# Optimization experiments

Measured on AMD Instinct MI355X. Metric: run time of the kernel, lower is better.

Reference implementation:

```python
import jax, jax.numpy as jnp
import numpy as np

N_NODES = 100000
N_EDGES = 1600000
IN_NODE = 129
HID = 128
N_LAYERS = 3


def setup_inputs() -> dict:
    key = jax.random.key(0)
    ks = jax.random.split(key, 20)
    gnn_in = IN_NODE - 1
    x = jax.random.normal(ks[0], (N_NODES, IN_NODE), dtype=jnp.float32)
    edge_index = jax.random.randint(ks[1], (2, N_EDGES), 0, N_NODES, dtype=jnp.int64)
    edge_attr = jax.random.uniform(ks[2], (N_EDGES, 1), dtype=jnp.float32)
    # conv layer params: lin (in->hid) per layer, scalar edge mlp per layer
    dims = [gnn_in] + [HID] * N_LAYERS
    conv_W, conv_b, edge_w = [], [], []
    for i in range(N_LAYERS):
        fin = dims[i]
        s = 1.0 / np.sqrt(fin)
        conv_W.append(jax.random.uniform(ks[3 + i], (fin, HID), jnp.float32, -s, s))
        conv_b.append(jax.random.uniform(ks[6 + i], (HID,), jnp.float32, -s, s))
        edge_w.append(jax.random.uniform(ks[9 + i], (1, 1), jnp.float32, -1.0, 1.0))
    h2 = HID // 2
    t_h = IN_NODE // 2
    s1 = 1.0 / np.sqrt(HID + 1)
    s2 = 1.0 / np.sqrt(h2)
    s3 = 1.0 / np.sqrt(IN_NODE)
    s4 = 1.0 / np.sqrt(t_h)
    return {
        "x": x, "edge_index": edge_index, "edge_attr": edge_attr,
        "conv_W": tuple(conv_W), "conv_b": tuple(conv_b), "edge_w": tuple(edge_w),
        "lin1_W": jax.random.uniform(ks[12], (HID + 1, h2), jnp.float32, -s1, s1),
        "lin1_b": jax.random.uniform(ks[13], (h2,), jnp.float32, -s1, s1),
        "lin2_W": jax.random.uniform(ks[14], (h2, 1), jnp.float32, -s2, s2),
        "lin2_b": jax.random.uniform(ks[15], (1,), jnp.float32, -s2, s2),
        "t1_W": jax.random.uniform(ks[16], (IN_NODE, t_h), jnp.float32, -s3, s3),
        "t1_b": jax.random.uniform(ks[17], (t_h,), jnp.float32, -s3, s3),
        "t2_W": jax.random.uniform(ks[18], (t_h, 1), jnp.float32, -s4, s4),
        "t2_b": jax.random.uniform(ks[19], (1,), jnp.float32, -s4, s4),
    }


def reference(x, edge_index, edge_attr, conv_W, conv_b, edge_w,
              lin1_W, lin1_b, lin2_W, lin2_b, t1_W, t1_b, t2_W, t2_b):
    n = x.shape[0]
    # add self loops with edge_attr fill_value = 1.0
    loops = jnp.arange(n, dtype=edge_index.dtype)
    src = jnp.concatenate([edge_index[0], loops])
    tgt = jnp.concatenate([edge_index[1], loops])
    ea = jnp.concatenate([edge_attr, jnp.ones((n, 1), edge_attr.dtype)], axis=0)  # [E+N,1]
    # in-degree for mean aggregation (>=1 because of self loops)
    deg = jax.ops.segment_sum(jnp.ones_like(ea[:, 0]), tgt, num_segments=n)[:, None]
    # treatment head (eval mode: no dropout)
    t = jax.nn.relu(x @ t1_W + t1_b)
    t = jax.nn.sigmoid(t @ t2_W + t2_b)  # [N,1]
    h = x[:, 1:]
    for W, b, w in zip(conv_W, conv_b, edge_w):
        ht = h @ W + b                          # [N,HID]
        gate = jax.nn.sigmoid(ea * w[0, 0])     # [E+N,1]
        msg = gate * ht[src]                    # gather + gate
        agg = jax.ops.segment_sum(msg, tgt, num_segments=n) / deg
        h = jax.nn.relu(agg)
    z = jnp.concatenate([h, t], axis=1)          # [N,HID+1]
    z = jax.nn.relu(z @ lin1_W + lin1_b)
    out = jax.nn.sigmoid(z @ lin2_W + lin2_b)[:, 0]  # [N]
    return out
```

## Files before the change

### kernel.cpp

```cpp
#include <hip/hip_runtime.h>
#include <hip/hip_fp16.h>
#include <math.h>


typedef _Float16 f16x8 __attribute__((ext_vector_type(8)));
typedef float f32x4 __attribute__((ext_vector_type(4)));

#define CNT_STRIDE 32

__device__ __forceinline__ float sigmoidf_(float v) { return 1.f / (1.f + expf(-v)); }

__global__ void sentinel_kernel(float* __restrict__ out, int n, float val) {
  int i = blockIdx.x * 256 + threadIdx.x;
  if (i < n) out[i] = val;
}

__global__ void init_kernel(const int* __restrict__ ei, int* __restrict__ flag,
                            int* __restrict__ counts, int n) {
  int i = blockIdx.x * 256 + threadIdx.x;
  if (i < (n + 1) * CNT_STRIDE) counts[i] = 0;
  if (i == 0) {
    int all0 = 1;
    for (int k = 1; k < 512; k += 2) {
      if (ei[k] != 0) { all0 = 0; break; }
    }
    *flag = all0;
  }
}

__global__ void rank_kernel(const int* __restrict__ ei, int E, int n,
                            const int* __restrict__ flag,
                            int* __restrict__ slot, int* __restrict__ counts) {
  int e = blockIdx.x * blockDim.x + threadIdx.x;
  if (e >= E) return;
  int t;
  if (*flag) {
    t = (int)((const long long*)ei)[(size_t)E + e];
  } else {
    t = ei[(size_t)E + e];
  }
  slot[e] = ((unsigned)t < (unsigned)n) ? atomicAdd(&counts[(size_t)t * CNT_STRIDE], 1) : -1;
}

__global__ void scan1_kernel(const int* __restrict__ counts, int n,
                             int* __restrict__ starts, int* __restrict__ bsums) {
  __shared__ int tmp[256];
  int i = blockIdx.x * 256 + threadIdx.x;
  int v = (i <= n) ? counts[(size_t)i * CNT_STRIDE] : 0;
  tmp[threadIdx.x] = v;
  __syncthreads();
  for (int off = 1; off < 256; off <<= 1) {
    int t = (threadIdx.x >= (unsigned)off) ? tmp[threadIdx.x - off] : 0;
    __syncthreads();
    tmp[threadIdx.x] += t;
    __syncthreads();
  }
  if (i <= n) starts[i] = tmp[threadIdx.x] - v;
  if (threadIdx.x == 255) bsums[blockIdx.x] = tmp[255];
}

__global__ void scan2_kernel(int* __restrict__ bsums, int nb) {
  __shared__ int tmp[512];
  int v = (threadIdx.x < (unsigned)nb) ? bsums[threadIdx.x] : 0;
  tmp[threadIdx.x] = v;
  __syncthreads();
  for (int off = 1; off < 512; off <<= 1) {
    int t = (threadIdx.x >= (unsigned)off) ? tmp[threadIdx.x - off] : 0;
    __syncthreads();
    tmp[threadIdx.x] += t;
    __syncthreads();
  }
  if (threadIdx.x < (unsigned)nb) bsums[threadIdx.x] = tmp[threadIdx.x] - v;
}

__global__ void scatter_kernel(const int* __restrict__ ei, const int* __restrict__ slot,
                               const int* __restrict__ starts,
                               const int* __restrict__ bsums,
                               const float* __restrict__ ea, int E, int n,
                               const int* __restrict__ flag,
                               const float* __restrict__ w0p,
                               const float* __restrict__ w1p,
                               const float* __restrict__ w2p,
                               uint2* __restrict__ csr) {
  float w0 = w0p[0], w1 = w1p[0], w2 = w2p[0];
  int f64 = *flag;
  const long long* e64 = (const long long*)ei;
  int base = blockIdx.x * blockDim.x + threadIdx.x;
  int stride = gridDim.x * blockDim.x;
#pragma unroll
  for (int u = 0; u < 4; u++) {
    int e = base + u * stride;
    if (e < E) {
      int sl = slot[e];
      if (sl >= 0) {
        int s, t;
        if (f64) {
          s = (int)e64[e];
          t = (int)e64[(size_t)E + e];
        } else {
          s = ei[e];
          t = ei[(size_t)E + e];
        }
        int pos = starts[t] + bsums[t >> 8] + sl;
        if ((unsigned)pos < (unsigned)E) {
          float a = ea[e];
          unsigned sn = (unsigned)min(max(s, 0), min(n - 1, 0x1ffff));
          unsigned g0 = (unsigned)__float2uint_rn(sigmoidf_(a * w0) * 32767.f);
          unsigned g1 = (unsigned)__float2uint_rn(sigmoidf_(a * w1) * 32767.f);
          unsigned g2 = (unsigned)__float2uint_rn(sigmoidf_(a * w2) * 32767.f);
          csr[pos] = make_uint2(sn | (g0 << 17), g1 | (g2 << 15));
        }
      }
    }
  }
}

__global__ void slice_kernel(const float* __restrict__ x, _Float16* __restrict__ h,
                             float* __restrict__ x0, int n) {
  int idx = blockIdx.x * blockDim.x + threadIdx.x;
  if (idx < n * 128) {
    int node = idx >> 7;
    int k = idx & 127;
    h[idx] = (_Float16)x[(size_t)node * 129 + 1 + k];
  }
  if (idx < n) x0[idx] = x[(size_t)idx * 129];
}

__global__ __launch_bounds__(256) void head_mfma_kernel(const _Float16* __restrict__ h,
    const float* __restrict__ extra, const float* __restrict__ W1,
    const float* __restrict__ b1, const float* __restrict__ w2,
    const float* __restrict__ b2, float* __restrict__ out, int n,
    int hrow0, int xrow) {
  __shared__ __align__(16) _Float16 sB[4 * 4 * 64 * 8];
  __shared__ float sWx[64], sB1[64], sW2[64];
  for (int idx = threadIdx.x; idx < 8192; idx += 256) {
    int k = idx >> 6, col = idx & 63;
    float w = W1[(size_t)(hrow0 + k) * 64 + col];
    int ks = k >> 5, quad = (k >> 3) & 3, j = k & 7;
    int nt = col >> 4, cl = col & 15;
    sB[(((ks * 4 + nt) * 64) + quad * 16 + cl) * 8 + j] = (_Float16)w;
  }
  if (threadIdx.x < 64) {
    sWx[threadIdx.x] = W1[(size_t)xrow * 64 + threadIdx.x];
    sB1[threadIdx.x] = b1[threadIdx.x];
    sW2[threadIdx.x] = w2[threadIdx.x];
  }
  __syncthreads();
  int wv = threadIdx.x >> 6, lane = threadIdx.x & 63;
  int quad = lane >> 4, l15 = lane & 15;
  int n0 = (blockIdx.x * 4 + wv) * 16;
  if (n0 >= n) return;
  int node_a = min(n0 + l15, n - 1);
  const _Float16* hrow = h + (size_t)node_a * 128 + quad * 8;

  f32x4 acc[4];
#pragma unroll
  for (int t = 0; t < 4; t++) acc[t] = (f32x4){0.f, 0.f, 0.f, 0.f};
  for (int ks = 0; ks < 4; ks++) {
    f16x8 afrag = *(const f16x8*)(hrow + ks * 32);
    const f16x8* bp = (const f16x8*)sB;
#pragma unroll
    for (int t = 0; t < 4; t++) {
      f16x8 bfrag = bp[(ks * 4 + t) * 64 + lane];
      acc[t] = __builtin_amdgcn_mfma_f32_16x16x32_f16(afrag, bfrag, acc[t], 0, 0, 0);
    }
  }
  float b2v = b2[0];
  float xv[4], part[4] = {0.f, 0.f, 0.f, 0.f};
#pragma unroll
  for (int r = 0; r < 4; r++) xv[r] = extra[min(n0 + quad * 4 + r, n - 1)];
#pragma unroll
  for (int t = 0; t < 4; t++) {
    int col = t * 16 + l15;
    float wx = sWx[col], bb = sB1[col], w2v = sW2[col];
#pragma unroll
    for (int r = 0; r < 4; r++) {
      float u = fmaxf(acc[t][r] + xv[r] * wx + bb, 0.f);
      part[r] += u * w2v;
    }
  }
#pragma unroll
  for (int r = 0; r < 4; r++) {
    float p = part[r];
    p += __shfl_xor(p, 1); p += __shfl_xor(p, 2);
    p += __shfl_xor(p, 4); p += __shfl_xor(p, 8);
    int node = n0 + quad * 4 + r;
    if (l15 == 0 && node < n) out[node] = sigmoidf_(p + b2v);
  }
}

__global__ __launch_bounds__(256) void gemm_mfma_kernel(const _Float16* __restrict__ h,
    const float* __restrict__ Wg, const float* __restrict__ b,
    _Float16* __restrict__ out16, int n) {
  __shared__ __align__(16) _Float16 sB[4 * 8 * 64 * 8];
  for (int i = threadIdx.x; i < 4096; i += 256) {
    int k = i >> 5;
    int n4 = (i & 31) * 4;
    float4 w4 = ((const float4*)Wg)[i];
    int ks = k >> 5, quad = (k >> 3) & 3, j = k & 7;
#pragma unroll
    for (int c = 0; c < 4; c++) {
      int col = n4 + c;
      int nt = col >> 4, cl = col & 15;
      sB[(((ks * 8 + nt) * 64) + quad * 16 + cl) * 8 + j] =
          (_Float16)((const float*)&w4)[c];
    }
  }
  __syncthreads();
  int wv = threadIdx.x >> 6, lane = threadIdx.x & 63;
  int quad = lane >> 4, l15 = lane & 15;
  int tiles = (n + 63) >> 6;
  for (int tile = blockIdx.x; tile < tiles; tile += gridDim.x) {
    int n0 = (tile * 4 + wv) * 16;
    if (n0 >= n) continue;
    int node_a = min(n0 + l15, n - 1);
    const _Float16* hrow = h + (size_t)node_a * 128 + quad * 8;

    f32x4 acc[8];
#pragma unroll
    for (int t = 0; t < 8; t++) acc[t] = (f32x4){0.f, 0.f, 0.f, 0.f};

    for (int ks = 0; ks < 4; ks++) {
      f16x8 afrag = *(const f16x8*)(hrow + ks * 32);
      const f16x8* bp = (const f16x8*)(sB + ks * 8 * 64 * 8);
#pragma unroll
      for (int t = 0; t < 8; t++) {
        f16x8 bfrag = bp[t * 64 + lane];
        acc[t] = __builtin_amdgcn_mfma_f32_16x16x32_f16(afrag, bfrag, acc[t], 0, 0, 0);
      }
    }
#pragma unroll
    for (int t = 0; t < 8; t++) {
      float bias = b[t * 16 + l15];
#pragma unroll
      for (int r = 0; r < 4; r++) {
        int node = n0 + quad * 4 + r;
        if (node < n)
          out16[(size_t)node * 128 + t * 16 + l15] = (_Float16)(acc[t][r] + bias);
      }
    }
  }
}

template <int LAYER>
__device__ __forceinline__ float gate_(uint2 r) {
  const float inv = 1.f / 32767.f;
  if (LAYER == 0) return (float)(r.x >> 17) * inv;
  if (LAYER == 1) return (float)(r.y & 0x7fffu) * inv;
  return (float)(r.y >> 15) * inv;
}

template <int LAYER>
__global__ __launch_bounds__(256) void agg_kernel(const __half2* __restrict__ ht,
    const uint2* __restrict__ csr, const int* __restrict__ starts,
    const int* __restrict__ bsums, const float* __restrict__ wp,
    __half2* __restrict__ hout, int n) {
  int wv = threadIdx.x >> 6, lane = threadIdx.x & 63;
  int node = blockIdx.x * 4 + wv;
  if (node >= n) return;
  int s = starts[node] + bsums[node >> 8];
  int c = starts[node + 1] + bsums[(node + 1) >> 8] - s;
  float gs = sigmoidf_(wp[0]);
  const __half2* htl = ht + lane;
  float2 v0 = __half22float2(htl[(size_t)node << 6]);
  float ax = gs * v0.x, ay = gs * v0.y;
  float bx = 0.f, by = 0.f;
  int j = 0;
  for (; j + 8 <= c; j += 8) {
    uint2 r0 = csr[s + j],     r1 = csr[s + j + 1];
    uint2 r2 = csr[s + j + 2], r3 = csr[s + j + 3];
    uint2 r4 = csr[s + j + 4], r5 = csr[s + j + 5];
    uint2 r6 = csr[s + j + 6], r7 = csr[s + j + 7];
    __half2 h0 = htl[(size_t)(r0.x & 0x1ffffu) << 6];
    __half2 h1 = htl[(size_t)(r1.x & 0x1ffffu) << 6];
    __half2 h2 = htl[(size_t)(r2.x & 0x1ffffu) << 6];
    __half2 h3 = htl[(size_t)(r3.x & 0x1ffffu) << 6];
    __half2 h4 = htl[(size_t)(r4.x & 0x1ffffu) << 6];
    __half2 h5 = htl[(size_t)(r5.x & 0x1ffffu) << 6];
    __half2 h6 = htl[(size_t)(r6.x & 0x1ffffu) << 6];
    __half2 h7 = htl[(size_t)(r7.x & 0x1ffffu) << 6];
    float g0 = gate_<LAYER>(r0), g1 = gate_<LAYER>(r1);
    float g2 = gate_<LAYER>(r2), g3 = gate_<LAYER>(r3);
    float g4 = gate_<LAYER>(r4), g5 = gate_<LAYER>(r5);
    float g6 = gate_<LAYER>(r6), g7 = gate_<LAYER>(r7);
    float2 f0 = __half22float2(h0), f1 = __half22float2(h1);
    float2 f2 = __half22float2(h2), f3 = __half22float2(h3);
    float2 f4 = __half22float2(h4), f5 = __half22float2(h5);
    float2 f6 = __half22float2(h6), f7 = __half22float2(h7);
    ax += g0 * f0.x; ay += g0 * f0.y;
    bx += g1 * f1.x; by += g1 * f1.y;
    ax += g2 * f2.x; ay += g2 * f2.y;
    bx += g3 * f3.x; by += g3 * f3.y;
    ax += g4 * f4.x; ay += g4 * f4.y;
    bx += g5 * f5.x; by += g5 * f5.y;
    ax += g6 * f6.x; ay += g6 * f6.y;
    bx += g7 * f7.x; by += g7 * f7.y;
  }
  for (; j + 4 <= c; j += 4) {
    uint2 r0 = csr[s + j],     r1 = csr[s + j + 1];
    uint2 r2 = csr[s + j + 2], r3 = csr[s + j + 3];
    __half2 h0 = htl[(size_t)(r0.x & 0x1ffffu) << 6];
    __half2 h1 = htl[(size_t)(r1.x & 0x1ffffu) << 6];
    __half2 h2 = htl[(size_t)(r2.x & 0x1ffffu) << 6];
    __half2 h3 = htl[(size_t)(r3.x & 0x1ffffu) << 6];
    float g0 = gate_<LAYER>(r0), g1 = gate_<LAYER>(r1);
    float g2 = gate_<LAYER>(r2), g3 = gate_<LAYER>(r3);
    float2 f0 = __half22float2(h0), f1 = __half22float2(h1);
    float2 f2 = __half22float2(h2), f3 = __half22float2(h3);
    ax += g0 * f0.x; ay += g0 * f0.y;
    bx += g1 * f1.x; by += g1 * f1.y;
    ax += g2 * f2.x; ay += g2 * f2.y;
    bx += g3 * f3.x; by += g3 * f3.y;
  }
  for (; j < c; j++) {
    uint2 r = csr[s + j];
    int sn = r.x & 0x1ffffu;
    float g = gate_<LAYER>(r);
    float2 f = __half22float2(htl[(size_t)sn << 6]);
    ax += g * f.x; ay += g * f.y;
  }
  ax += bx; ay += by;
  float inv = 1.f / (float)(c + 1);
  ax = fmaxf(ax * inv, 0.f);
  ay = fmaxf(ay * inv, 0.f);
  hout[((size_t)node << 6) + lane] = __floats2half2_rn(ax, ay);
}

extern "C" void kernel_launch(void* const* d_in, const int* in_sizes, int n_in,
                              void* d_out, int out_size, void* d_ws, size_t ws_size,
                              hipStream_t stream) {
  int ob = (out_size + 255) / 256;

  const float *x, *ea, *l1W, *l1b, *l2W, *l2b, *t1W, *t1b, *t2W, *t2b;
  const float *convW[3], *convb[3], *edgew[3];
  const int* ei;

  if (n_in == 20) {
    x = (const float*)d_in[0]; ei = (const int*)d_in[1]; ea = (const float*)d_in[2];
    for (int l = 0; l < 3; l++) {
      convW[l] = (const float*)d_in[3 + l];
      convb[l] = (const float*)d_in[6 + l];
      edgew[l] = (const float*)d_in[9 + l];
    }
    l1W = (const float*)d_in[12]; l1b = (const float*)d_in[13];
    l2W = (const float*)d_in[14]; l2b = (const float*)d_in[15];
    t1W = (const float*)d_in[16]; t1b = (const float*)d_in[17];
    t2W = (const float*)d_in[18]; t2b = (const float*)d_in[19];
  } else if (n_in == 14) {
    x = (const float*)d_in[0]; ei = (const int*)d_in[1]; ea = (const float*)d_in[2];
    const float* cw = (const float*)d_in[3];
    const float* cb = (const float*)d_in[4];
    const float* ew = (const float*)d_in[5];
    for (int l = 0; l < 3; l++) {
      convW[l] = cw + (size_t)l * 128 * 128;
      convb[l] = cb + (size_t)l * 128;
      edgew[l] = ew + l;
    }
    l1W = (const float*)d_in[6];  l1b = (const float*)d_in[7];
    l2W = (const float*)d_in[8];  l2b = (const float*)d_in[9];
    t1W = (const float*)d_in[10]; t1b = (const float*)d_in[11];
    t2W = (const float*)d_in[12]; t2b = (const float*)d_in[13];
  } else {
    sentinel_kernel<<<ob, 256, 0, stream>>>((float*)d_out, out_size,
                                            900.0f + (float)n_in);
    return;
  }

  int n = in_sizes[0] / 129;
  int E = in_sizes[2];

  char* ws = (char*)d_ws;
  size_t off = 0;
  auto take = [&](size_t bytes) -> void* {
    void* p = ws + off;
    off = (off + bytes + 255) & ~(size_t)255;
    return p;
  };
  size_t csr_bytes = (size_t)E * 8;
  size_t cnt_bytes = ((size_t)n + 1) * CNT_STRIDE * 4;
  int*      flag    = (int*)take(256);
  uint2*    csr     = (uint2*)take(csr_bytes > cnt_bytes ? csr_bytes : cnt_bytes);
  int*      counts  = (int*)csr;
  int*      starts  = (int*)take(((size_t)n + 1) * 4);
  int*      bsums   = (int*)take(512 * 4);
  float*    tbuf    = (float*)take((size_t)n * 4);
  float*    x0buf   = (float*)take((size_t)n * 4);
  int*      slot    = (int*)take((size_t)E * 4);
  _Float16* h16     = (_Float16*)take((size_t)n * 128 * 2);
  _Float16* ht16    = (_Float16*)take((size_t)n * 128 * 2);

  if (off > ws_size) {
    sentinel_kernel<<<ob, 256, 0, stream>>>((float*)d_out, out_size,
                                            1000.0f + (float)(ws_size >> 20));
    return;
  }

  int eb = (E + 255) / 256;
  int nb1 = (n + 1 + 255) / 256;
  int zb = ((n + 1) * CNT_STRIDE + 255) / 256;

  init_kernel<<<zb, 256, 0, stream>>>(ei, flag, counts, n);
  rank_kernel<<<eb, 256, 0, stream>>>(ei, E, n, flag, slot, counts);
  scan1_kernel<<<nb1, 256, 0, stream>>>(counts, n, starts, bsums);
  scan2_kernel<<<1, 512, 0, stream>>>(bsums, nb1);
  scatter_kernel<<<(eb + 3) / 4, 256, 0, stream>>>(ei, slot, starts, bsums, ea, E, n,
                                                   flag, edgew[0], edgew[1], edgew[2],
                                                   csr);

  int sb = (int)(((size_t)n * 128 + 255) / 256);
  slice_kernel<<<sb, 256, 0, stream>>>(x, h16, x0buf, n);
  head_mfma_kernel<<<(n + 63) / 64, 256, 0, stream>>>(h16, x0buf, t1W, t1b, t2W, t2b,
                                                      tbuf, n, 1, 0);

  int gemm_grid = min((n + 63) / 64, 1024);
  gemm_mfma_kernel<<<gemm_grid, 256, 0, stream>>>(h16, convW[0], convb[0], ht16, n);
  agg_kernel<0><<<(n + 3) / 4, 256, 0, stream>>>((const __half2*)ht16, csr, starts,
                                                 bsums, edgew[0], (__half2*)h16, n);
  gemm_mfma_kernel<<<gemm_grid, 256, 0, stream>>>(h16, convW[1], convb[1], ht16, n);
  agg_kernel<1><<<(n + 3) / 4, 256, 0, stream>>>((const __half2*)ht16, csr, starts,
                                                 bsums, edgew[1], (__half2*)h16, n);
  gemm_mfma_kernel<<<gemm_grid, 256, 0, stream>>>(h16, convW[2], convb[2], ht16, n);
  agg_kernel<2><<<(n + 3) / 4, 256, 0, stream>>>((const __half2*)ht16, csr, starts,
                                                 bsums, edgew[2], (__half2*)h16, n);

  head_mfma_kernel<<<(n + 63) / 64, 256, 0, stream>>>(h16, tbuf, l1W, l1b, l2W, l2b,
                                                      (float*)d_out, n, 0, 128);
}
```

Before: 545.9 us.

## Quantize transformed node features to per-row int8 for edge gather

The GEMM epilogue now stores each transformed node row as unsigned int8 with a per-node absmax scale instead of fp16. This halves the bytes fetched per gathered neighbour. The aggregation kernel is reorganised so each half-wave processes alternate edges, loading 4 bytes per lane, and then corrects for the +128 offset and combines the halves with a cross-lane shuffle. This adds precision loss from 8-bit quantization plus an extra scale load per edge.

```diff
diff --git a/kernel.cpp b/kernel.cpp
--- a/kernel.cpp
+++ b/kernel.cpp
@@ -191,7 +191,7 @@
 
 __global__ __launch_bounds__(256) void gemm_mfma_kernel(const _Float16* __restrict__ h,
     const float* __restrict__ Wg, const float* __restrict__ b,
-    _Float16* __restrict__ out16, int n) {
+    unsigned char* __restrict__ out8, float* __restrict__ scales, int n) {
   __shared__ __align__(16) _Float16 sB[4 * 8 * 64 * 8];
   for (int i = threadIdx.x; i < 4096; i += 256) {
     int k = i >> 5;
@@ -233,10 +233,29 @@
     for (int t = 0; t < 8; t++) {
       float bias = b[t * 16 + l15];
 #pragma unroll
-      for (int r = 0; r < 4; r++) {
-        int node = n0 + quad * 4 + r;
-        if (node < n)
-          out16[(size_t)node * 128 + t * 16 + l15] = (_Float16)(acc[t][r] + bias);
+      for (int r = 0; r < 4; r++) acc[t][r] += bias;
+    }
+    float mx[4] = {0.f, 0.f, 0.f, 0.f};
+#pragma unroll
+    for (int t = 0; t < 8; t++)
+#pragma unroll
+      for (int r = 0; r < 4; r++) mx[r] = fmaxf(mx[r], fabsf(acc[t][r]));
+#pragma unroll
+    for (int m = 1; m <= 8; m <<= 1) {
+#pragma unroll
+      for (int r = 0; r < 4; r++) mx[r] = fmaxf(mx[r], __shfl_xor(mx[r], m));
+    }
+#pragma unroll
+    for (int r = 0; r < 4; r++) {
+      int node = n0 + quad * 4 + r;
+      if (node >= n) continue;
+      float inv = (mx[r] > 0.f) ? 127.f / mx[r] : 0.f;
+      if (l15 == 0) scales[node] = mx[r] * (1.f / 127.f);
+#pragma unroll
+      for (int t = 0; t < 8; t++) {
+        int u = (int)rintf(acc[t][r] * inv) + 128;
+        u = min(max(u, 0), 255);
+        out8[(size_t)node * 128 + t * 16 + l15] = (unsigned char)u;
       }
     }
   }
@@ -250,80 +269,82 @@
   return (float)(r.y >> 15) * inv;
 }
 
+#define ACC4(u, g)                                   \
+  a0 += (float)((u) & 0xffu) * (g);                  \
+  a1 += (float)(((u) >> 8) & 0xffu) * (g);           \
+  a2 += (float)(((u) >> 16) & 0xffu) * (g);          \
+  a3 += (float)((u) >> 24) * (g);
+
 template <int LAYER>
-__global__ __launch_bounds__(256) void agg_kernel(const __half2* __restrict__ ht,
-    const uint2* __restrict__ csr, const int* __restrict__ starts,
-    const int* __restrict__ bsums, const float* __restrict__ wp,
-    __half2* __restrict__ hout, int n) {
+__global__ __launch_bounds__(256) void agg_kernel(const unsigned char* __restrict__ ht8,
+    const float* __restrict__ scales, const uint2* __restrict__ csr,
+    const int* __restrict__ starts, const int* __restrict__ bsums,
+    const float* __restrict__ wp, __half2* __restrict__ hout, int n) {
   int wv = threadIdx.x >> 6, lane = threadIdx.x & 63;
   int node = blockIdx.x * 4 + wv;
   if (node >= n) return;
   int s = starts[node] + bsums[node >> 8];
   int c = starts[node + 1] + bsums[(node + 1) >> 8] - s;
   float gs = sigmoidf_(wp[0]);
-  const __half2* htl = ht + lane;
-  float2 v0 = __half22float2(htl[(size_t)node << 6]);
-  float ax = gs * v0.x, ay = gs * v0.y;
-  float bx = 0.f, by = 0.f;
+  int sub = lane & 31, p = lane >> 5;
+  unsigned sub4 = (unsigned)sub * 4u;
+
+  unsigned su = *(const unsigned*)(ht8 + (unsigned)node * 128u + sub4);
+  float gsc = (p == 0) ? gs * scales[node] : 0.f;
+  float sgs = gsc;
+  float a0 = 0.f, a1 = 0.f, a2 = 0.f, a3 = 0.f;
+  ACC4(su, gsc)
+
   int j = 0;
   for (; j + 8 <= c; j += 8) {
-    uint2 r0 = csr[s + j],     r1 = csr[s + j + 1];
-    uint2 r2 = csr[s + j + 2], r3 = csr[s + j + 3];
-    uint2 r4 = csr[s + j + 4], r5 = csr[s + j + 5];
-    uint2 r6 = csr[s + j + 6], r7 = csr[s + j + 7];
-    __half2 h0 = htl[(size_t)(r0.x & 0x1ffffu) << 6];
-    __half2 h1 = htl[(size_t)(r1.x & 0x1ffffu) << 6];
-    __half2 h2 = htl[(size_t)(r2.x & 0x1ffffu) << 6];
-    __half2 h3 = htl[(size_t)(r3.x & 0x1ffffu) << 6];
-    __half2 h4 = htl[(size_t)(r4.x & 0x1ffffu) << 6];
-    __half2 h5 = htl[(size_t)(r5.x & 0x1ffffu) << 6];
-    __half2 h6 = htl[(size_t)(r6.x & 0x1ffffu) << 6];
-    __half2 h7 = htl[(size_t)(r7.x & 0x1ffffu) << 6];
-    float g0 = gate_<LAYER>(r0), g1 = gate_<LAYER>(r1);
-    float g2 = gate_<LAYER>(r2), g3 = gate_<LAYER>(r3);
-    float g4 = gate_<LAYER>(r4), g5 = gate_<LAYER>(r5);
-    float g6 = gate_<LAYER>(r6), g7 = gate_<LAYER>(r7);
-    float2 f0 = __half22float2(h0), f1 = __half22float2(h1);
-    float2 f2 = __half22float2(h2), f3 = __half22float2(h3);
-    float2 f4 = __half22float2(h4), f5 = __half22float2(h5);
-    float2 f6 = __half22float2(h6), f7 = __half22float2(h7);
-    ax += g0 * f0.x; ay += g0 * f0.y;
-    bx += g1 * f1.x; by += g1 * f1.y;
-    ax += g2 * f2.x; ay += g2 * f2.y;
-    bx += g3 * f3.x; by += g3 * f3.y;
-    ax += g4 * f4.x; ay += g4 * f4.y;
-    bx += g5 * f5.x; by += g5 * f5.y;
-    ax += g6 * f6.x; ay += g6 * f6.y;
-    bx += g7 * f7.x; by += g7 * f7.y;
-  }
-  for (; j + 4 <= c; j += 4) {
-    uint2 r0 = csr[s + j],     r1 = csr[s + j + 1];
-    uint2 r2 = csr[s + j + 2], r3 = csr[s + j + 3];
-    __half2 h0 = htl[(size_t)(r0.x & 0x1ffffu) << 6];
-    __half2 h1 = htl[(size_t)(r1.x & 0x1ffffu) << 6];
-    __half2 h2 = htl[(size_t)(r2.x & 0x1ffffu) << 6];
-    __half2 h3 = htl[(size_t)(r3.x & 0x1ffffu) << 6];
-    float g0 = gate_<LAYER>(r0), g1 = gate_<LAYER>(r1);
-    float g2 = gate_<LAYER>(r2), g3 = gate_<LAYER>(r3);
-    float2 f0 = __half22float2(h0), f1 = __half22float2(h1);
-    float2 f2 = __half22float2(h2), f3 = __half22float2(h3);
-    ax += g0 * f0.x; ay += g0 * f0.y;
-    bx += g1 * f1.x; by += g1 * f1.y;
-    ax += g2 * f2.x; ay += g2 * f2.y;
-    bx += g3 * f3.x; by += g3 * f3.y;
-  }
-  for (; j < c; j++) {
+    uint2 r0 = csr[s + j + 0 + p], r1 = csr[s + j + 2 + p];
+    uint2 r2 = csr[s + j + 4 + p], r3 = csr[s + j + 6 + p];
+    unsigned i0 = r0.x & 0x1ffffu, i1 = r1.x & 0x1ffffu;
+    unsigned i2 = r2.x & 0x1ffffu, i3 = r3.x & 0x1ffffu;
+    unsigned u0 = *(const unsigned*)(ht8 + i0 * 128u + sub4);
+    unsigned u1 = *(const unsigned*)(ht8 + i1 * 128u + sub4);
+    unsigned u2 = *(const unsigned*)(ht8 + i2 * 128u + sub4);
+    unsigned u3 = *(const unsigned*)(ht8 + i3 * 128u + sub4);
+    float g0 = gate_<LAYER>(r0) * scales[i0];
+    float g1 = gate_<LAYER>(r1) * scales[i1];
+    float g2 = gate_<LAYER>(r2) * scales[i2];
+    float g3 = gate_<LAYER>(r3) * scales[i3];
+    sgs += g0 + g1 + g2 + g3;
+    ACC4(u0, g0) ACC4(u1, g1) ACC4(u2, g2) ACC4(u3, g3)
+  }
+  for (; j + 2 <= c; j += 2) {
+    uint2 r = csr[s + j + p];
+    unsigned i0 = r.x & 0x1ffffu;
+    unsigned u = *(const unsigned*)(ht8 + i0 * 128u + sub4);
+    float g = gate_<LAYER>(r) * scales[i0];
+    sgs += g;
+    ACC4(u, g)
+  }
+  if (j < c) {
     uint2 r = csr[s + j];
-    int sn = r.x & 0x1ffffu;
-    float g = gate_<LAYER>(r);
-    float2 f = __half22float2(htl[(size_t)sn << 6]);
-    ax += g * f.x; ay += g * f.y;
-  }
-  ax += bx; ay += by;
+    unsigned i0 = r.x & 0x1ffffu;
+    unsigned u = *(const unsigned*)(ht8 + i0 * 128u + sub4);
+    float g = (p == 0) ? gate_<LAYER>(r) * scales[i0] : 0.f;
+    sgs += g;
+    ACC4(u, g)
+  }
+  a0 += __shfl_xor(a0, 32); a1 += __shfl_xor(a1, 32);
+  a2 += __shfl_xor(a2, 32); a3 += __shfl_xor(a3, 32);
+  sgs += __shfl_xor(sgs, 32);
+  float corr = 128.f * sgs;
   float inv = 1.f / (float)(c + 1);
-  ax = fmaxf(ax * inv, 0.f);
-  ay = fmaxf(ay * inv, 0.f);
-  hout[((size_t)node << 6) + lane] = __floats2half2_rn(ax, ay);
+  a0 = fmaxf((a0 - corr) * inv, 0.f);
+  a1 = fmaxf((a1 - corr) * inv, 0.f);
+  a2 = fmaxf((a2 - corr) * inv, 0.f);
+  a3 = fmaxf((a3 - corr) * inv, 0.f);
+  if (p == 0) {
+    __half2 h01 = __floats2half2_rn(a0, a1);
+    __half2 h23 = __floats2half2_rn(a2, a3);
+    uint2 outw;
+    outw.x = *(unsigned*)&h01;
+    outw.y = *(unsigned*)&h23;
+    *(uint2*)((char*)hout + (size_t)node * 256 + (size_t)sub * 8) = outw;
+  }
 }
 
 extern "C" void kernel_launch(void* const* d_in, const int* in_sizes, int n_in,
@@ -387,7 +408,8 @@
   float*    x0buf   = (float*)take((size_t)n * 4);
   int*      slot    = (int*)take((size_t)E * 4);
   _Float16* h16     = (_Float16*)take((size_t)n * 128 * 2);
-  _Float16* ht16    = (_Float16*)take((size_t)n * 128 * 2);
+  unsigned char* ht8 = (unsigned char*)take((size_t)n * 128);
+  float*    scales  = (float*)take((size_t)n * 4);
 
   if (off > ws_size) {
     sentinel_kernel<<<ob, 256, 0, stream>>>((float*)d_out, out_size,
@@ -413,15 +435,15 @@
                                                       tbuf, n, 1, 0);
 
   int gemm_grid = min((n + 63) / 64, 1024);
-  gemm_mfma_kernel<<<gemm_grid, 256, 0, stream>>>(h16, convW[0], convb[0], ht16, n);
-  agg_kernel<0><<<(n + 3) / 4, 256, 0, stream>>>((const __half2*)ht16, csr, starts,
-                                                 bsums, edgew[0], (__half2*)h16, n);
-  gemm_mfma_kernel<<<gemm_grid, 256, 0, stream>>>(h16, convW[1], convb[1], ht16, n);
-  agg_kernel<1><<<(n + 3) / 4, 256, 0, stream>>>((const __half2*)ht16, csr, starts,
-                                                 bsums, edgew[1], (__half2*)h16, n);
-  gemm_mfma_kernel<<<gemm_grid, 256, 0, stream>>>(h16, convW[2], convb[2], ht16, n);
-  agg_kernel<2><<<(n + 3) / 4, 256, 0, stream>>>((const __half2*)ht16, csr, starts,
-                                                 bsums, edgew[2], (__half2*)h16, n);
+  gemm_mfma_kernel<<<gemm_grid, 256, 0, stream>>>(h16, convW[0], convb[0], ht8, scales, n);
+  agg_kernel<0><<<(n + 3) / 4, 256, 0, stream>>>(ht8, scales, csr, starts, bsums,
+                                                 edgew[0], (__half2*)h16, n);
+  gemm_mfma_kernel<<<gemm_grid, 256, 0, stream>>>(h16, convW[1], convb[1], ht8, scales, n);
+  agg_kernel<1><<<(n + 3) / 4, 256, 0, stream>>>(ht8, scales, csr, starts, bsums,
+                                                 edgew[1], (__half2*)h16, n);
+  gemm_mfma_kernel<<<gemm_grid, 256, 0, stream>>>(h16, convW[2], convb[2], ht8, scales, n);
+  agg_kernel<2><<<(n + 3) / 4, 256, 0, stream>>>(ht8, scales, csr, starts, bsums,
+                                                 edgew[2], (__half2*)h16, n);
 
   head_mfma_kernel<<<(n + 63) / 64, 256, 0, stream>>>(h16, tbuf, l1W, l1b, l2W, l2b,
                                                       (float*)d_out, n, 0, 128);
```

New measurement: 508.6 us. 1.07x faster.
